# Kernel tuning notes

Measured on AMD Instinct MI355X. Metric: run time of the kernel, lower is better.

Reference implementation:

```python
import jax, jax.numpy as jnp
import numpy as np

B, T, I, H, L = 256, 256, 256, 1024, 128


def setup_inputs() -> dict:
    key = jax.random.key(0)
    ks = jax.random.split(key, 10)
    s = 0.05
    return {
        "z": jax.random.normal(ks[0], (B, L), dtype=jnp.float32),
        "seq_len": T,
        "target": jax.random.uniform(ks[1], (B, T, I), dtype=jnp.float32),
        "W_z2h": jax.random.normal(ks[2], (H, L), dtype=jnp.float32) * s,
        "b_z2h": jnp.zeros((H,), dtype=jnp.float32),
        "W_ih": jax.random.normal(ks[3], (3 * H, I), dtype=jnp.float32) * s,
        "W_hh": jax.random.normal(ks[4], (3 * H, H), dtype=jnp.float32) * s,
        "b_ih": jnp.zeros((3 * H,), dtype=jnp.float32),
        "b_hh": jnp.zeros((3 * H,), dtype=jnp.float32),
        "W_out": jax.random.normal(ks[5], (I, H), dtype=jnp.float32) * s,
        "b_out": jnp.zeros((I,), dtype=jnp.float32),
    }


def reference(z, seq_len, target, W_z2h, b_z2h, W_ih, W_hh, b_ih, b_hh, W_out, b_out):
    # h0 = tanh(Linear(z))  -- [B, H]
    h0 = jnp.tanh(z @ W_z2h.T + b_z2h)
    # Precompute input-side gate pre-activations for all steps: [T, B, 3H]
    xg = jnp.einsum("bti,gi->tbg", target, W_ih) + b_ih

    hdim = h0.shape[-1]

    def step(h, xg_t):
        hg = h @ W_hh.T + b_hh  # [B, 3H]
        xr, xz, xn = jnp.split(xg_t, 3, axis=-1)
        hr, hz, hn = jnp.split(hg, 3, axis=-1)
        r = jax.nn.sigmoid(xr + hr)
        zg = jax.nn.sigmoid(xz + hz)
        n = jnp.tanh(xn + r * hn)
        h_new = (1.0 - zg) * n + zg * h
        y = jax.nn.sigmoid(h_new @ W_out.T + b_out)  # [B, I]
        return h_new, y

    _, ys = jax.lax.scan(step, h0, xg)  # ys: [T, B, I]
    return jnp.transpose(ys, (1, 0, 2))  # [B, T, I]
```

## Files before the change

### kernel.cpp

```cpp
#include <hip/hip_runtime.h>

#define BB 256
#define TT 256
#define II 256
#define HH 1024
#define LL 128
#define K1 1280
#define GN 3072

typedef short s8v    __attribute__((ext_vector_type(8)));
typedef float f32x4  __attribute__((ext_vector_type(4)));
typedef float f4v    __attribute__((ext_vector_type(4)));

__device__ __forceinline__ unsigned short f2bf(float f) {
    unsigned u = __float_as_uint(f);
    u += 0x7fffu + ((u >> 16) & 1u);
    return (unsigned short)(u >> 16);
}
__device__ __forceinline__ float bf2f(unsigned short h) {
    return __uint_as_float(((unsigned)h) << 16);
}
__device__ __forceinline__ float sigm(float x) { return 1.0f / (1.0f + __expf(-x)); }

__device__ __forceinline__ s8v cvt8(const float* __restrict__ p) {
    const f4v lo = *(const f4v*)p;
    const f4v hi = *(const f4v*)(p + 4);
    s8v r;
    r[0] = (short)f2bf(lo[0]); r[1] = (short)f2bf(lo[1]);
    r[2] = (short)f2bf(lo[2]); r[3] = (short)f2bf(lo[3]);
    r[4] = (short)f2bf(hi[0]); r[5] = (short)f2bf(hi[1]);
    r[6] = (short)f2bf(hi[2]); r[7] = (short)f2bf(hi[3]);
    return r;
}

__global__ void k_prep_w(const float* __restrict__ Whh, const float* __restrict__ Wih,
                         unsigned short* __restrict__ Wperm) {
    int o = blockIdx.x;
    int ntt = o / 48, q = o - ntt * 48;
    int gate = q >> 4, j = ntt * 16 + (q & 15);
    int src = gate * HH + j;
    const float* sh = Whh + (size_t)src * HH;
    const float* si = Wih + (size_t)src * II;
    unsigned short* dst = Wperm + (size_t)o * K1;
    for (int k = threadIdx.x; k < K1; k += 256)
        dst[k] = f2bf(k < HH ? sh[k] : si[k - HH]);
}

__global__ void k_prep_misc(const float* __restrict__ bih, const float* __restrict__ bhh,
                            const float* __restrict__ Wout,
                            float* __restrict__ bihp, float* __restrict__ bhhp,
                            unsigned short* __restrict__ Woutb) {
    int idx = blockIdx.x * 256 + threadIdx.x;
    if (idx < GN) {
        int ntt = idx / 48, q = idx - ntt * 48;
        int gate = q >> 4, j = ntt * 16 + (q & 15);
        int src = gate * HH + j;
        bihp[idx] = bih[src];
        bhhp[idx] = bhh[src];
    }
    for (size_t i = (size_t)blockIdx.x * 256 + threadIdx.x; i < (size_t)II * HH;
         i += (size_t)gridDim.x * 256)
        Woutb[i] = f2bf(Wout[i]);
}

__global__ void k_h0(const float* __restrict__ z, const float* __restrict__ Wz,
                     const float* __restrict__ bz, unsigned short* __restrict__ hbuf) {
    int b = blockIdx.x >> 2;
    int j = ((blockIdx.x & 3) << 8) + threadIdx.x;
    const f4v* zr = (const f4v*)(z + (size_t)b * LL);
    const f4v* wr = (const f4v*)(Wz + (size_t)j * LL);
    float s = bz[j];
#pragma unroll
    for (int i = 0; i < LL / 4; ++i) {
        f4v a = zr[i], w = wr[i];
        s += a[0] * w[0] + a[1] * w[1] + a[2] * w[2] + a[3] * w[3];
    }
    hbuf[(size_t)b * HH + j] = f2bf(tanhf(s));
}

__device__ __forceinline__ void proj_tile(
    const unsigned short* __restrict__ hb, const unsigned short* __restrict__ Woutb,
    float* __restrict__ out, float (*pred)[256],
    int bo, int io, int wave, int lane, int lr, int lk, int tp, float boutv) {
    f32x4 oa = {0.f, 0.f, 0.f, 0.f};
    const unsigned short* ap = hb + (size_t)(bo * 16 + lr) * HH + (wave << 8) + lk;
    const unsigned short* wp = Woutb + (size_t)(io * 16 + lr) * HH + (wave << 8) + lk;
#pragma unroll
    for (int ks = 0; ks < 8; ++ks) {
        s8v a = *(const s8v*)(ap + ks * 32);
        s8v w = *(const s8v*)(wp + ks * 32);
        oa = __builtin_amdgcn_mfma_f32_16x16x32_bf16(a, w, oa, 0, 0, 0);
    }
    if (wave >= 1) {
#pragma unroll
        for (int r = 0; r < 4; ++r)
            pred[wave - 1][(((lane >> 4) << 2) + r) * 16 + lr] = oa[r];
    }
    __syncthreads();
    if (wave == 0) {
#pragma unroll
        for (int r = 0; r < 4; ++r) {
            int rw = ((lane >> 4) << 2) + r;
            int idx = rw * 16 + lr;
            float v = oa[r] + pred[0][idx] + pred[1][idx] + pred[2][idx] + boutv;
            out[(size_t)(bo * 16 + rw) * (TT * II) + (size_t)tp * II + io * 16 + lr] = sigm(v);
        }
    }
}

__global__ __launch_bounds__(256, 1) void dec_main(
    const float* __restrict__ tgt,
    const unsigned short* __restrict__ Wperm,
    const float* __restrict__ bihp, const float* __restrict__ bhhp,
    unsigned short* __restrict__ hbuf,
    const unsigned short* __restrict__ Woutb,
    const float* __restrict__ bout,
    float* __restrict__ out,
    unsigned* __restrict__ barr) {
    __shared__ float red[3][3072];
    __shared__ float gxn[1024];
    __shared__ float pred[3][256];

    const int tid = threadIdx.x;
    const int wave = tid >> 6, lane = tid & 63;
    const int lr = lane & 15;
    const int lk = (lane >> 4) << 3;
    const int bid = blockIdx.x;
    const int m = bid >> 6, nt = bid & 63;
    const int bo = (m << 2) + (nt >> 4), io = nt & 15;

    const int ejj = tid & 15;
    const int ob = nt * 48;
    const float bi_r  = bihp[ob + ejj] + bhhp[ob + ejj];
    const float bi_z  = bihp[ob + 16 + ejj] + bhhp[ob + 16 + ejj];
    const float bi_xn = bihp[ob + 32 + ejj];
    const float bi_hn = bhhp[ob + 32 + ejj];
    const float boutv = bout[io * 16 + lr];

    unsigned* mybarr = barr + m * TT;

    for (int t = 0; t < TT; ++t) {
        const unsigned short* hcur = hbuf + (size_t)(t % 3) * (BB * HH);
        unsigned short* hnxt = hbuf + (size_t)((t + 1) % 3) * (BB * HH);

        f32x4 acc[12];
#pragma unroll
        for (int i = 0; i < 12; ++i) acc[i] = (f32x4){0.f, 0.f, 0.f, 0.f};

        if (wave < 3) {
            const int kb = wave * 320;
            const unsigned short* hp0 = hcur + (size_t)(m * 64 + lr) * HH + kb + lk;
            const unsigned short* wp0 = Wperm + (size_t)(nt * 48 + lr) * K1 + kb + lk;
#pragma unroll
            for (int ks = 0; ks < 10; ++ks) {
                s8v a[4], w[3];
#pragma unroll
                for (int mi = 0; mi < 4; ++mi)
                    a[mi] = *(const s8v*)(hp0 + (size_t)mi * 16 * HH + ks * 32);
#pragma unroll
                for (int ni = 0; ni < 3; ++ni)
                    w[ni] = *(const s8v*)(wp0 + (size_t)ni * 16 * K1 + ks * 32);
#pragma unroll
                for (int mi = 0; mi < 4; ++mi)
#pragma unroll
                    for (int ni = 0; ni < 3; ++ni)
                        acc[mi * 3 + ni] = __builtin_amdgcn_mfma_f32_16x16x32_bf16(
                            a[mi], w[ni], acc[mi * 3 + ni], 0, 0, 0);
            }
        } else {
            f32x4 accx[4];
#pragma unroll
            for (int i = 0; i < 4; ++i) accx[i] = (f32x4){0.f, 0.f, 0.f, 0.f};
            {
                const unsigned short* hp0 = hcur + (size_t)(m * 64 + lr) * HH + 960 + lk;
                const unsigned short* wp0 = Wperm + (size_t)(nt * 48 + lr) * K1 + 960 + lk;
#pragma unroll
                for (int ks = 0; ks < 2; ++ks) {
                    s8v a[4], w[3];
#pragma unroll
                    for (int mi = 0; mi < 4; ++mi)
                        a[mi] = *(const s8v*)(hp0 + (size_t)mi * 16 * HH + ks * 32);
#pragma unroll
                    for (int ni = 0; ni < 3; ++ni)
                        w[ni] = *(const s8v*)(wp0 + (size_t)ni * 16 * K1 + ks * 32);
#pragma unroll
                    for (int mi = 0; mi < 4; ++mi)
#pragma unroll
                        for (int ni = 0; ni < 3; ++ni)
                            acc[mi * 3 + ni] = __builtin_amdgcn_mfma_f32_16x16x32_bf16(
                                a[mi], w[ni], acc[mi * 3 + ni], 0, 0, 0);
                }
            }
            {
                const float* xp0 = tgt + ((size_t)(m * 64 + lr) * TT + t) * II + lk;
                const unsigned short* wp0 = Wperm + (size_t)(nt * 48 + lr) * K1 + HH + lk;
#pragma unroll
                for (int ks = 0; ks < 8; ++ks) {
                    s8v a[4], w[3];
#pragma unroll
                    for (int mi = 0; mi < 4; ++mi)
                        a[mi] = cvt8(xp0 + (size_t)mi * 16 * TT * II + ks * 32);
#pragma unroll
                    for (int ni = 0; ni < 3; ++ni)
                        w[ni] = *(const s8v*)(wp0 + (size_t)ni * 16 * K1 + ks * 32);
#pragma unroll
                    for (int mi = 0; mi < 4; ++mi) {
                        acc[mi * 3 + 0] = __builtin_amdgcn_mfma_f32_16x16x32_bf16(a[mi], w[0], acc[mi * 3 + 0], 0, 0, 0);
                        acc[mi * 3 + 1] = __builtin_amdgcn_mfma_f32_16x16x32_bf16(a[mi], w[1], acc[mi * 3 + 1], 0, 0, 0);
                        accx[mi]        = __builtin_amdgcn_mfma_f32_16x16x32_bf16(a[mi], w[2], accx[mi], 0, 0, 0);
                    }
                }
            }
#pragma unroll
            for (int mi = 0; mi < 4; ++mi)
#pragma unroll
                for (int r = 0; r < 4; ++r)
                    gxn[(mi * 16 + ((lane >> 4) << 2) + r) * 16 + lr] = accx[mi][r];
        }

        if (wave >= 1) {
            float* s = &red[wave - 1][0];
#pragma unroll
            for (int mi = 0; mi < 4; ++mi)
#pragma unroll
                for (int ni = 0; ni < 3; ++ni)
#pragma unroll
                    for (int r = 0; r < 4; ++r)
                        s[(mi * 16 + ((lane >> 4) << 2) + r) * 48 + ni * 16 + lr] =
                            acc[mi * 3 + ni][r];
        }
        __syncthreads();
        if (wave == 0) {
#pragma unroll
            for (int mi = 0; mi < 4; ++mi)
#pragma unroll
                for (int ni = 0; ni < 3; ++ni)
#pragma unroll
                    for (int r = 0; r < 4; ++r) {
                        int idx = (mi * 16 + ((lane >> 4) << 2) + r) * 48 + ni * 16 + lr;
                        red[0][idx] = acc[mi * 3 + ni][r] + red[0][idx] + red[1][idx] + red[2][idx];
                    }
        }
        __syncthreads();

        {
            const int b0t = tid >> 4;
#pragma unroll
            for (int it = 0; it < 4; ++it) {
                int b = b0t + it * 16;
                float ghr = red[0][b * 48 + ejj];
                float ghz = red[0][b * 48 + 16 + ejj];
                float ghn = red[0][b * 48 + 32 + ejj];
                float gx  = gxn[b * 16 + ejj];
                float r   = sigm(ghr + bi_r);
                float zg  = sigm(ghz + bi_z);
                float n   = tanhf(gx + bi_xn + r * (ghn + bi_hn));
                int bg = m * 64 + b, jg = nt * 16 + ejj;
                float hold = bf2f(hcur[(size_t)bg * HH + jg]);
                hnxt[(size_t)bg * HH + jg] = f2bf((1.f - zg) * n + zg * hold);
            }
        }

        __syncthreads();
        if (tid == 0)
            __hip_atomic_fetch_add(mybarr + t, 1u, __ATOMIC_RELEASE, __HIP_MEMORY_SCOPE_AGENT);

        if (t > 0)
            proj_tile(hcur, Woutb, out, pred, bo, io, wave, lane, lr, lk, t - 1, boutv);

        if (tid == 0) {
            int guard = 0;
            while (__hip_atomic_load(mybarr + t, __ATOMIC_RELAXED,
                                     __HIP_MEMORY_SCOPE_AGENT) < 64u) {
                __builtin_amdgcn_s_sleep(1);
                if (++guard > (1 << 17)) break;
            }
            __builtin_amdgcn_fence(__ATOMIC_ACQUIRE, "agent");
        }
        __syncthreads();
    }
    proj_tile(hbuf + (size_t)(TT % 3) * (BB * HH), Woutb, out, pred,
              bo, io, wave, lane, lr, lk, TT - 1, boutv);
}

extern "C" void kernel_launch(void* const* d_in, const int* in_sizes, int n_in,
                              void* d_out, int out_size, void* d_ws, size_t ws_size,
                              hipStream_t stream) {
    const float* z    = (const float*)d_in[0];
    const float* tgt  = (const float*)d_in[2];
    const float* Wz2h = (const float*)d_in[3];
    const float* bz2h = (const float*)d_in[4];
    const float* Wih  = (const float*)d_in[5];
    const float* Whh  = (const float*)d_in[6];
    const float* bih  = (const float*)d_in[7];
    const float* bhh  = (const float*)d_in[8];
    const float* Wout = (const float*)d_in[9];
    const float* bout = (const float*)d_in[10];
    float* out = (float*)d_out;

    char* ws = (char*)d_ws;
    unsigned short* Wperm = (unsigned short*)ws;
    float* bihp           = (float*)(ws + 7864320);
    float* bhhp           = (float*)(ws + 7876608);
    unsigned short* Woutb = (unsigned short*)(ws + 7888896);
    unsigned short* hbuf  = (unsigned short*)(ws + 8413184);
    unsigned* barr        = (unsigned*)(ws + 9986048);

    hipMemsetAsync(barr, 0, 4 * TT * sizeof(unsigned), stream);
    hipLaunchKernelGGL(k_prep_w, dim3(GN), dim3(256), 0, stream, Whh, Wih, Wperm);
    hipLaunchKernelGGL(k_prep_misc, dim3(1024), dim3(256), 0, stream, bih, bhh, Wout,
                       bihp, bhhp, Woutb);
    hipLaunchKernelGGL(k_h0, dim3(BB * 4), dim3(256), 0, stream, z, Wz2h, bz2h, hbuf);
    hipLaunchKernelGGL(dec_main, dim3(256), dim3(256), 0, stream,
                       tgt, Wperm, bihp, bhhp, hbuf, Woutb, bout, out, barr);
}
```

Before: 5.395 ms.

## Replace acquire fences with relaxed device-scope atomics and pad LDS tiles

Hidden-state reads and writes now go through relaxed agent-scope 64-bit atomic loads and stores. The acquire fence and release ordering on the per-step barrier are dropped, and a waitcnt before the barrier increment takes their place, to avoid full cache invalidation or writeback on every step. The GRU elementwise stage is reorganized so each thread handles 4 contiguous hidden units and stores them packed. The reduction, gx and projection LDS buffers get padded strides to cut bank conflicts. The change relies on relaxed atomics bypassing non-coherent caches, which risks memory-ordering correctness and may slow the 16-byte hidden loads by splitting them into two 8-byte atomics.

```diff
diff --git a/kernel.cpp b/kernel.cpp
--- a/kernel.cpp
+++ b/kernel.cpp
@@ -8,9 +8,14 @@
 #define K1 1280
 #define GN 3072
 
+#define RP 52
+#define GP 20
+#define PP 20
+
 typedef short s8v    __attribute__((ext_vector_type(8)));
 typedef float f32x4  __attribute__((ext_vector_type(4)));
 typedef float f4v    __attribute__((ext_vector_type(4)));
+typedef unsigned long long u64;
 
 __device__ __forceinline__ unsigned short f2bf(float f) {
     unsigned u = __float_as_uint(f);
@@ -21,6 +26,19 @@
     return __uint_as_float(((unsigned)h) << 16);
 }
 __device__ __forceinline__ float sigm(float x) { return 1.0f / (1.0f + __expf(-x)); }
+
+__device__ __forceinline__ u64 hload8(const unsigned short* p) {
+    return __hip_atomic_load((const u64*)p, __ATOMIC_RELAXED, __HIP_MEMORY_SCOPE_AGENT);
+}
+__device__ __forceinline__ s8v hload16(const unsigned short* p) {
+    union { u64 q[2]; s8v v; } u;
+    u.q[0] = __hip_atomic_load((const u64*)p, __ATOMIC_RELAXED, __HIP_MEMORY_SCOPE_AGENT);
+    u.q[1] = __hip_atomic_load((const u64*)p + 1, __ATOMIC_RELAXED, __HIP_MEMORY_SCOPE_AGENT);
+    return u.v;
+}
+__device__ __forceinline__ void hstore8(unsigned short* p, u64 v) {
+    __hip_atomic_store((u64*)p, v, __ATOMIC_RELAXED, __HIP_MEMORY_SCOPE_AGENT);
+}
 
 __device__ __forceinline__ s8v cvt8(const float* __restrict__ p) {
     const f4v lo = *(const f4v*)p;
@@ -65,43 +83,49 @@
 
 __global__ void k_h0(const float* __restrict__ z, const float* __restrict__ Wz,
                      const float* __restrict__ bz, unsigned short* __restrict__ hbuf) {
-    int b = blockIdx.x >> 2;
-    int j = ((blockIdx.x & 3) << 8) + threadIdx.x;
+    int b = blockIdx.x;
+    int j0 = threadIdx.x * 4;
     const f4v* zr = (const f4v*)(z + (size_t)b * LL);
-    const f4v* wr = (const f4v*)(Wz + (size_t)j * LL);
-    float s = bz[j];
-#pragma unroll
-    for (int i = 0; i < LL / 4; ++i) {
-        f4v a = zr[i], w = wr[i];
-        s += a[0] * w[0] + a[1] * w[1] + a[2] * w[2] + a[3] * w[3];
-    }
-    hbuf[(size_t)b * HH + j] = f2bf(tanhf(s));
+    u64 packed = 0;
+#pragma unroll
+    for (int jj = 0; jj < 4; ++jj) {
+        int j = j0 + jj;
+        const f4v* wr = (const f4v*)(Wz + (size_t)j * LL);
+        float s = bz[j];
+#pragma unroll
+        for (int i = 0; i < LL / 4; ++i) {
+            f4v a = zr[i], w = wr[i];
+            s += a[0] * w[0] + a[1] * w[1] + a[2] * w[2] + a[3] * w[3];
+        }
+        packed |= (u64)f2bf(tanhf(s)) << (16 * jj);
+    }
+    hstore8(hbuf + (size_t)b * HH + j0, packed);
 }
 
 __device__ __forceinline__ void proj_tile(
     const unsigned short* __restrict__ hb, const unsigned short* __restrict__ Woutb,
-    float* __restrict__ out, float (*pred)[256],
+    float* __restrict__ out, float (*pred)[16 * PP],
     int bo, int io, int wave, int lane, int lr, int lk, int tp, float boutv) {
     f32x4 oa = {0.f, 0.f, 0.f, 0.f};
     const unsigned short* ap = hb + (size_t)(bo * 16 + lr) * HH + (wave << 8) + lk;
     const unsigned short* wp = Woutb + (size_t)(io * 16 + lr) * HH + (wave << 8) + lk;
 #pragma unroll
     for (int ks = 0; ks < 8; ++ks) {
-        s8v a = *(const s8v*)(ap + ks * 32);
+        s8v a = hload16(ap + ks * 32);
         s8v w = *(const s8v*)(wp + ks * 32);
         oa = __builtin_amdgcn_mfma_f32_16x16x32_bf16(a, w, oa, 0, 0, 0);
     }
     if (wave >= 1) {
 #pragma unroll
         for (int r = 0; r < 4; ++r)
-            pred[wave - 1][(((lane >> 4) << 2) + r) * 16 + lr] = oa[r];
+            pred[wave - 1][(((lane >> 4) << 2) + r) * PP + lr] = oa[r];
     }
     __syncthreads();
     if (wave == 0) {
 #pragma unroll
         for (int r = 0; r < 4; ++r) {
             int rw = ((lane >> 4) << 2) + r;
-            int idx = rw * 16 + lr;
+            int idx = rw * PP + lr;
             float v = oa[r] + pred[0][idx] + pred[1][idx] + pred[2][idx] + boutv;
             out[(size_t)(bo * 16 + rw) * (TT * II) + (size_t)tp * II + io * 16 + lr] = sigm(v);
         }
@@ -117,9 +141,9 @@
     const float* __restrict__ bout,
     float* __restrict__ out,
     unsigned* __restrict__ barr) {
-    __shared__ float red[3][3072];
-    __shared__ float gxn[1024];
-    __shared__ float pred[3][256];
+    __shared__ float red[3][64 * RP];
+    __shared__ float gxn[64 * GP];
+    __shared__ float pred[3][16 * PP];
 
     const int tid = threadIdx.x;
     const int wave = tid >> 6, lane = tid & 63;
@@ -129,12 +153,18 @@
     const int m = bid >> 6, nt = bid & 63;
     const int bo = (m << 2) + (nt >> 4), io = nt & 15;
 
-    const int ejj = tid & 15;
+    const int eb = tid & 63;
+    const int ej4 = (tid >> 6) << 2;
     const int ob = nt * 48;
-    const float bi_r  = bihp[ob + ejj] + bhhp[ob + ejj];
-    const float bi_z  = bihp[ob + 16 + ejj] + bhhp[ob + 16 + ejj];
-    const float bi_xn = bihp[ob + 32 + ejj];
-    const float bi_hn = bhhp[ob + 32 + ejj];
+    float bir[4], biz[4], bixn[4], bihn[4];
+#pragma unroll
+    for (int jj = 0; jj < 4; ++jj) {
+        int j = ej4 + jj;
+        bir[jj]  = bihp[ob + j] + bhhp[ob + j];
+        biz[jj]  = bihp[ob + 16 + j] + bhhp[ob + 16 + j];
+        bixn[jj] = bihp[ob + 32 + j];
+        bihn[jj] = bhhp[ob + 32 + j];
+    }
     const float boutv = bout[io * 16 + lr];
 
     unsigned* mybarr = barr + m * TT;
@@ -156,7 +186,7 @@
                 s8v a[4], w[3];
 #pragma unroll
                 for (int mi = 0; mi < 4; ++mi)
-                    a[mi] = *(const s8v*)(hp0 + (size_t)mi * 16 * HH + ks * 32);
+                    a[mi] = hload16(hp0 + (size_t)mi * 16 * HH + ks * 32);
 #pragma unroll
                 for (int ni = 0; ni < 3; ++ni)
                     w[ni] = *(const s8v*)(wp0 + (size_t)ni * 16 * K1 + ks * 32);
@@ -179,7 +209,7 @@
                     s8v a[4], w[3];
 #pragma unroll
                     for (int mi = 0; mi < 4; ++mi)
-                        a[mi] = *(const s8v*)(hp0 + (size_t)mi * 16 * HH + ks * 32);
+                        a[mi] = hload16(hp0 + (size_t)mi * 16 * HH + ks * 32);
 #pragma unroll
                     for (int ni = 0; ni < 3; ++ni)
                         w[ni] = *(const s8v*)(wp0 + (size_t)ni * 16 * K1 + ks * 32);
@@ -215,7 +245,7 @@
             for (int mi = 0; mi < 4; ++mi)
 #pragma unroll
                 for (int r = 0; r < 4; ++r)
-                    gxn[(mi * 16 + ((lane >> 4) << 2) + r) * 16 + lr] = accx[mi][r];
+                    gxn[(mi * 16 + ((lane >> 4) << 2) + r) * GP + lr] = accx[mi][r];
         }
 
         if (wave >= 1) {
@@ -226,7 +256,7 @@
                 for (int ni = 0; ni < 3; ++ni)
 #pragma unroll
                     for (int r = 0; r < 4; ++r)
-                        s[(mi * 16 + ((lane >> 4) << 2) + r) * 48 + ni * 16 + lr] =
+                        s[(mi * 16 + ((lane >> 4) << 2) + r) * RP + ni * 16 + lr] =
                             acc[mi * 3 + ni][r];
         }
         __syncthreads();
@@ -237,33 +267,38 @@
                 for (int ni = 0; ni < 3; ++ni)
 #pragma unroll
                     for (int r = 0; r < 4; ++r) {
-                        int idx = (mi * 16 + ((lane >> 4) << 2) + r) * 48 + ni * 16 + lr;
+                        int idx = (mi * 16 + ((lane >> 4) << 2) + r) * RP + ni * 16 + lr;
                         red[0][idx] = acc[mi * 3 + ni][r] + red[0][idx] + red[1][idx] + red[2][idx];
                     }
         }
         __syncthreads();
 
         {
-            const int b0t = tid >> 4;
-#pragma unroll
-            for (int it = 0; it < 4; ++it) {
-                int b = b0t + it * 16;
-                float ghr = red[0][b * 48 + ejj];
-                float ghz = red[0][b * 48 + 16 + ejj];
-                float ghn = red[0][b * 48 + 32 + ejj];
-                float gx  = gxn[b * 16 + ejj];
-                float r   = sigm(ghr + bi_r);
-                float zg  = sigm(ghz + bi_z);
-                float n   = tanhf(gx + bi_xn + r * (ghn + bi_hn));
-                int bg = m * 64 + b, jg = nt * 16 + ejj;
-                float hold = bf2f(hcur[(size_t)bg * HH + jg]);
-                hnxt[(size_t)bg * HH + jg] = f2bf((1.f - zg) * n + zg * hold);
-            }
-        }
-
+            const int bg = m * 64 + eb;
+            const int jbase = nt * 16 + ej4;
+            u64 hold8 = hload8(hcur + (size_t)bg * HH + jbase);
+            u64 packed = 0;
+#pragma unroll
+            for (int jj = 0; jj < 4; ++jj) {
+                int c = ej4 + jj;
+                float ghr = red[0][eb * RP + c];
+                float ghz = red[0][eb * RP + 16 + c];
+                float ghn = red[0][eb * RP + 32 + c];
+                float gx  = gxn[eb * GP + c];
+                float r   = sigm(ghr + bir[jj]);
+                float zg  = sigm(ghz + biz[jj]);
+                float n   = tanhf(gx + bixn[jj] + r * (ghn + bihn[jj]));
+                float hold = bf2f((unsigned short)(hold8 >> (16 * jj)));
+                float hnew = (1.f - zg) * n + zg * hold;
+                packed |= (u64)f2bf(hnew) << (16 * jj);
+            }
+            hstore8(hnxt + (size_t)bg * HH + jbase, packed);
+        }
+
+        asm volatile("s_waitcnt vmcnt(0)" ::: "memory");
         __syncthreads();
         if (tid == 0)
-            __hip_atomic_fetch_add(mybarr + t, 1u, __ATOMIC_RELEASE, __HIP_MEMORY_SCOPE_AGENT);
+            __hip_atomic_fetch_add(mybarr + t, 1u, __ATOMIC_RELAXED, __HIP_MEMORY_SCOPE_AGENT);
 
         if (t > 0)
             proj_tile(hcur, Woutb, out, pred, bo, io, wave, lane, lr, lk, t - 1, boutv);
@@ -275,7 +310,6 @@
                 __builtin_amdgcn_s_sleep(1);
                 if (++guard > (1 << 17)) break;
             }
-            __builtin_amdgcn_fence(__ATOMIC_ACQUIRE, "agent");
         }
         __syncthreads();
     }
@@ -310,7 +344,7 @@
     hipLaunchKernelGGL(k_prep_w, dim3(GN), dim3(256), 0, stream, Whh, Wih, Wperm);
     hipLaunchKernelGGL(k_prep_misc, dim3(1024), dim3(256), 0, stream, bih, bhh, Wout,
                        bihp, bhhp, Woutb);
-    hipLaunchKernelGGL(k_h0, dim3(BB * 4), dim3(256), 0, stream, z, Wz2h, bz2h, hbuf);
+    hipLaunchKernelGGL(k_h0, dim3(BB), dim3(256), 0, stream, z, Wz2h, bz2h, hbuf);
     hipLaunchKernelGGL(dec_main, dim3(256), dim3(256), 0, stream,
                        tgt, Wperm, bihp, bhhp, hbuf, Woutb, bout, out, barr);
 }
```

Result: faster. 5.286 ms (-2.0%).
